# Optimization experiments

Measured on AMD Instinct MI355X. Metric: run time of the kernel, lower is better.

## Reference

```python
import jax, jax.numpy as jnp
import numpy as np

EPS = 1e-6

def rms_norm(x, w):
    # x: (..., hd), w: (hd,)
    norm = jax.lax.rsqrt(jnp.mean(x * x, axis=-1, keepdims=True) + EPS)
    return x * norm * w

def rotate_half(x):
    x1, x2 = jnp.split(x, 2, axis=-1)
    return jnp.concatenate((-x2, x1), axis=-1)

def setup_inputs() -> dict:
    key = jax.random.key(0)
    ks = jax.random.split(key, 5)
    B, L, C, H = 8, 1024, 1024, 16
    hd = C // H
    x = jax.random.normal(ks[0], (B, L, C), dtype=jnp.float32)
    # RoPE tables (realistic: derived from angles; any broadcastable table works)
    pos = jnp.arange(L, dtype=jnp.float32)[:, None]
    inv_freq = 1.0 / (10000.0 ** (jnp.arange(0, hd, 2, dtype=jnp.float32) / hd))
    ang = pos * inv_freq[None, :]              # (L, hd/2)
    ang = jnp.concatenate([ang, ang], axis=-1) # (L, hd)
    cos = jnp.cos(ang)
    sin = jnp.sin(ang)
    w_qkv = jax.random.normal(ks[1], (3 * C, C), dtype=jnp.float32) * (C ** -0.5)
    w_proj = jax.random.normal(ks[2], (C, C), dtype=jnp.float32) * (C ** -0.5)
    q_norm_w = jnp.ones((hd,), dtype=jnp.float32)
    k_norm_w = jnp.ones((hd,), dtype=jnp.float32)
    return {"x": x, "cos": cos, "sin": sin, "w_qkv": w_qkv, "w_proj": w_proj,
            "q_norm_w": q_norm_w, "k_norm_w": k_norm_w}

def reference(x, cos, sin, w_qkv, w_proj, q_norm_w, k_norm_w):
    B, L, C = x.shape
    H = 16
    hd = C // H
    # qkv: torch Linear(bias=False) -> x @ W^T, W: (3C, C)
    qkv = jnp.einsum('blc,dc->bld', x, w_qkv)             # (B, L, 3C)
    qkv = qkv.reshape(B, L, 3, H, hd).transpose(2, 0, 3, 1, 4)  # (3, B, H, L, hd)
    q, k, v = qkv[0], qkv[1], qkv[2]
    q = rms_norm(q, q_norm_w)
    k = rms_norm(k, k_norm_w)
    # RoPE: cos/sin (L, hd) broadcast over (B, H, L, hd)
    q = q * cos + rotate_half(q) * sin
    k = k * cos + rotate_half(k) * sin
    scale = 1.0 / np.sqrt(hd).astype(np.float32)
    attn = jnp.einsum('bhqd,bhkd->bhqk', q, k) * scale    # (B, H, L, L)
    attn = jax.nn.softmax(attn, axis=-1)
    out = jnp.einsum('bhqk,bhkd->bhqd', attn, v)          # (B, H, L, hd)
    out = out.transpose(0, 2, 1, 3).reshape(B, L, C)
    return jnp.einsum('blc,dc->bld', out, w_proj)
```

## Files before the change

kernel.cpp:

```cpp
#include <hip/hip_runtime.h>
#include <hip/hip_bf16.h>
#include <stdint.h>

typedef uint16_t u16;
typedef uint32_t u32;
typedef __attribute__((ext_vector_type(8))) short bv8;
typedef __attribute__((ext_vector_type(4))) float f32x4;
typedef __attribute__((ext_vector_type(16))) float f32x16;
typedef __attribute__((ext_vector_type(2))) u32 u32x2;

#define MFMA(a,b,c)   __builtin_amdgcn_mfma_f32_16x16x32_bf16((a),(b),(c),0,0,0)
#define MFMA32(a,b,c) __builtin_amdgcn_mfma_f32_32x32x16_bf16((a),(b),(c),0,0,0)

__device__ __forceinline__ float bf2f(u16 v){ u32 x=(u32)v<<16; float f; __builtin_memcpy(&f,&x,4); return f; }
__device__ __forceinline__ u16 f2bf(float f){ u32 x; __builtin_memcpy(&x,&f,4); x += 0x7fffu + ((x>>16)&1u); return (u16)(x>>16); }
__device__ __forceinline__ u32 cvtpk_bf16(float lo, float hi){
  u32 r; asm("v_cvt_pk_bf16_f32 %0, %1, %2" : "=v"(r) : "v"(lo), "v"(hi)); return r;
}
__device__ __forceinline__ float exp2_fast(float x){
  float r; asm("v_exp_f32 %0, %1" : "=v"(r) : "v"(x)); return r;
}
__device__ __forceinline__ float rcp_fast(float x){
  float r; asm("v_rcp_f32 %0, %1" : "=v"(r) : "v"(x)); return r;
}

__device__ __forceinline__ void gl_lds16(const u16* g, u16* l){
  __builtin_amdgcn_global_load_lds((const __attribute__((address_space(1))) u32*)g,
                                   (__attribute__((address_space(3))) u32*)l, 16, 0, 0);
}

__global__ __launch_bounds__(256) void cvt3(const float* __restrict__ x, const float* __restrict__ wq,
                                            const float* __restrict__ wp, u16* __restrict__ dst){
  const long NA = 1048576, NB = 393216, NC = 131072;
  long i = (long)blockIdx.x*256 + threadIdx.x;
  long stride = (long)gridDim.x*256;
  for(; i < NA+NB+NC; i += stride){
    const float* s;
    if(i < NA)            s = x  + i*8;
    else if(i < NA+NB)    s = wq + (i-NA)*8;
    else                  s = wp + (i-NA-NB)*8;
    f32x4 a = *(const f32x4*)(s);
    f32x4 b = *(const f32x4*)(s + 4);
    bv8 o;
    #pragma unroll
    for(int j=0;j<4;j++) o[j]   = (short)f2bf(a[j]);
    #pragma unroll
    for(int j=0;j<4;j++) o[4+j] = (short)f2bf(b[j]);
    *(bv8*)(dst + i*8) = o;
  }
}

template<int MODE>
__global__ __launch_bounds__(256,2) void gemm_bt(const u16* __restrict__ A, const u16* __restrict__ B,
                                                 void* __restrict__ Cv, int M, int N, int K,
                                                 const float* __restrict__ cosT,
                                                 const float* __restrict__ sinT,
                                                 const float* __restrict__ qw,
                                                 const float* __restrict__ kw){
  __shared__ __align__(16) u16 As[128*64];
  __shared__ __align__(16) u16 Bs[128*64];
  int nwg = gridDim.x;
  int wg  = (int)blockIdx.x;
  wg = (wg & 7)*(nwg>>3) + (wg>>3);
  int nn = N>>7;
  int tm = wg/nn, tn = wg - tm*nn;
  int rowbase = tm<<7, colbase = tn<<7;
  int t = threadIdx.x, lane = t&63, w = t>>6;
  int g = lane>>4, q16 = lane&15;
  int wr = w>>1, wc = w&1;

  f32x4 z = {0.f,0.f,0.f,0.f};
  f32x4 acc[4][4];
  #pragma unroll
  for(int i=0;i<4;i++)
    #pragma unroll
    for(int j=0;j<4;j++) acc[i][j]=z;

  for(int k0=0;k0<K;k0+=64){
    __syncthreads();
    #pragma unroll
    for(int i=0;i<4;i++){
      int s = ((w<<2)+i)*64 + lane;
      int row = s>>3;
      int ksl = (s&7) ^ (row&7);
      gl_lds16(A + (size_t)(rowbase+row)*K + k0 + ksl*8, (u16*)As + ((w<<2)+i)*512);
      gl_lds16(B + (size_t)(colbase+row)*K + k0 + ksl*8, (u16*)Bs + ((w<<2)+i)*512);
    }
    __syncthreads();
    #pragma unroll
    for(int eks=0;eks<2;eks++){
      bv8 af[4], bfr[4];
      #pragma unroll
      for(int mi=0;mi<4;mi++){
        int row = (wr<<6)+(mi<<4)+q16;
        af[mi] = *(const bv8*)(As + row*64 + ((((eks<<2)|g) ^ (row&7))<<3));
      }
      #pragma unroll
      for(int ni=0;ni<4;ni++){
        int row = (wc<<6)+(ni<<4)+q16;
        bfr[ni] = *(const bv8*)(Bs + row*64 + ((((eks<<2)|g) ^ (row&7))<<3));
      }
      #pragma unroll
      for(int mi=0;mi<4;mi++)
        #pragma unroll
        for(int ni=0;ni<4;ni++)
          acc[mi][ni] = MFMA(af[mi], bfr[ni], acc[mi][ni]);
    }
  }

  if(MODE==2 && colbase < 2048){
    int s = colbase>>10;
    const float* wsel = s ? kw : qw;
    int ch = colbase + (wc<<6);
    float qsc = s ? 1.0f : 0.1803368801111437f;
    float wv[4];
    #pragma unroll
    for(int ni=0;ni<4;ni++) wv[ni] = wsel[(ni<<4)|q16];
    #pragma unroll
    for(int mi=0;mi<4;mi++){
      #pragma unroll
      for(int r=0;r<4;r++){
        int row = rowbase + (wr<<6)+(mi<<4)+(g<<2)+r;
        int l = row & 1023;
        float y[4];
        float ss = 0.f;
        #pragma unroll
        for(int ni=0;ni<4;ni++){ y[ni]=acc[mi][ni][r]; ss += y[ni]*y[ni]; }
        ss += __shfl_xor(ss,1,64); ss += __shfl_xor(ss,2,64);
        ss += __shfl_xor(ss,4,64); ss += __shfl_xor(ss,8,64);
        float nrm = rsqrtf(ss*(1.f/64.f) + 1e-6f);
        #pragma unroll
        for(int ni=0;ni<4;ni++) y[ni] *= nrm * wv[ni];
        u16* cp = (u16*)Cv + (size_t)row*N + ch;
        #pragma unroll
        for(int ni=0;ni<4;ni++){
          int d = (ni<<4)|q16;
          float rot = (ni<2) ? -y[ni+2] : y[ni-2];
          float o = (y[ni]*cosT[l*64+d] + rot*sinT[l*64+d]) * qsc;
          cp[d] = f2bf(o);
        }
      }
    }
    return;
  }

  #pragma unroll
  for(int mi=0;mi<4;mi++){
    #pragma unroll
    for(int ni=0;ni<4;ni++){
      int row = rowbase + (wr<<6) + (mi<<4) + (g<<2);
      int col = colbase + (wc<<6) + (ni<<4) + q16;
      if(MODE==1){
        float* cp = (float*)Cv + (size_t)row*N + col;
        #pragma unroll
        for(int r=0;r<4;r++) cp[(size_t)r*N] = acc[mi][ni][r];
      } else {
        u16* cp = (u16*)Cv + (size_t)row*N + col;
        #pragma unroll
        for(int r=0;r<4;r++) cp[(size_t)r*N] = f2bf(acc[mi][ni][r]);
      }
    }
  }
}

__global__ __launch_bounds__(512,1) void fattn(const u16* __restrict__ qkv, u16* __restrict__ Out){
  __shared__ __align__(16) u16 Ks0[128*64];
  __shared__ __align__(16) u16 Ks1[128*64];
  __shared__ __align__(16) u16 Vt[2][64*128];

  int t = threadIdx.x, lane = t&63, w = t>>6;
  int ql = lane&31, h = lane>>5;
  int nwg = gridDim.x;
  int bid = (int)blockIdx.x;
  bid = (bid & 7)*(nwg>>3) + (bid>>3);
  int bh = bid >> 2, qt = bid & 3;
  int b = bh >> 4, hd = bh & 15;
  const u16* base = qkv + (size_t)b*1024*3072;
  int Qb = (qt<<8) + (w<<5);

  bv8 qf[4];
  {
    const u16* qp = base + (size_t)(Qb+ql)*3072 + hd*64 + (h<<3);
    qf[0] = *(const bv8*)(qp);
    qf[1] = *(const bv8*)(qp+16);
    qf[2] = *(const bv8*)(qp+32);
    qf[3] = *(const bv8*)(qp+48);
  }
  bv8 onesb;
  #pragma unroll
  for(int j=0;j<8;j++) onesb[j] = (short)0x3F80;

  f32x16 accO0, accO1, accL;
  #pragma unroll
  for(int r=0;r<16;r++){ accO0[r]=0.f; accO1[r]=0.f; accL[r]=0.f; }
  float m_run = -1e30f;

  bool vstage = (t < 256);
  int d0v = (t&7)<<3;
  int c4  = (t>>3)&31;
  int sV = c4>>1, halfV = c4&1, kvr = c4<<2;
  int d15b = (t&1)<<3;
  int vxt  = ((t>>1)&3)<<1;

  bv8 v0,v1,v2,v3;
  const u16* gV0 = base + (size_t)kvr*3072 + 2048 + hd*64 + d0v;

#define LDV(tl) if(vstage){ const u16* gV = gV0 + (size_t)(tl)*393216; \
    v0 = *(const bv8*)(gV);       v1 = *(const bv8*)(gV+3072); \
    v2 = *(const bv8*)(gV+6144);  v3 = *(const bv8*)(gV+9216); }

#define STV(buf) if(vstage){ \
    _Pragma("unroll") \
    for(int i=0;i<8;i++){ \
      int d = d0v + i; \
      u32x2 val; \
      val.x = (u32)(u16)v0[i] | ((u32)(u16)v1[i]<<16); \
      val.y = (u32)(u16)v2[i] | ((u32)(u16)v3[i]<<16); \
      *(u32x2*)((buf) + d*128 + ((((sV ^ (d15b+i) ^ vxt))<<3) + (halfV<<2))) = val; \
    } }

#define KDMA(tl, buf) { \
    _Pragma("unroll") \
    for(int i=0;i<2;i++){ \
      int si = ((w<<1)+i)*64 + lane; \
      int row = si>>3; \
      int esl = (si&7) ^ (row&7); \
      gl_lds16(base + (size_t)(((tl)<<7)+row)*3072 + 1024 + hd*64 + esl*8, (buf) + ((w<<1)+i)*512); \
    } }

  KDMA(0, (u16*)Ks0);
  LDV(0);
  STV(Vt[0]);
  LDV(1);

  int rx0 = (ql>>4)<<1;
  int dsw = ql & 15;

  for(int tile=0; tile<8; ++tile){
    u16* kcur = (tile&1) ? (u16*)Ks1 : (u16*)Ks0;
    u16* knxt = (tile&1) ? (u16*)Ks0 : (u16*)Ks1;
    u16* vcur = Vt[tile&1];
    u16* vnxt = Vt[(tile&1)^1];
    __syncthreads();
    if(tile<7) KDMA(tile+1, knxt);

    #pragma unroll
    for(int sub=0; sub<2; ++sub){
      f32x16 s0, s1;
      #pragma unroll
      for(int r=0;r<16;r++){ s0[r]=0.f; s1[r]=0.f; }
      int rowA = (sub<<6) + ql;
      int rowB = rowA + 32;
      __builtin_amdgcn_s_setprio(1);
      #pragma unroll
      for(int s=0;s<4;s++){
        bv8 ka = *(const bv8*)(kcur + rowA*64 + ((((s<<1)|h) ^ (rowA&7))<<3));
        bv8 kb = *(const bv8*)(kcur + rowB*64 + ((((s<<1)|h) ^ (rowB&7))<<3));
        s0 = MFMA32(ka, qf[s], s0);
        s1 = MFMA32(kb, qf[s], s1);
      }
      __builtin_amdgcn_s_setprio(0);

      if(sub==0){
        if(tile<7) STV(vnxt);
        if(tile<6) LDV(tile+2);
      }

      float rm = -1e30f;
      #pragma unroll
      for(int r=0;r<16;r++){ rm = fmaxf(rm, fmaxf(s0[r], s1[r])); }
      rm = fmaxf(rm, __shfl_xor(rm, 32, 64));
      if(__any(rm > m_run + 8.0f)){
        float mnew = fmaxf(m_run, rm);
        float fac = exp2_fast(m_run - mnew);
        m_run = mnew;
        #pragma unroll
        for(int r=0;r<16;r++){
          int qs = (r&3) + ((r>>2)<<3) + (h<<2);
          float fr = __shfl(fac, qs, 64);
          accO0[r] *= fr; accO1[r] *= fr; accL[r] *= fr;
        }
      }
      #pragma unroll
      for(int r=0;r<16;r++){
        s0[r] = exp2_fast(s0[r]-m_run);
        s1[r] = exp2_fast(s1[r]-m_run);
      }

      #pragma unroll
      for(int tt=0; tt<4; ++tt){
        int b0 = (tt&1)<<1;
        float a0,a1,a2,a3,b4,b5,b6,b7;
        if(tt<2){ a0=s0[4*b0+0]; a1=s0[4*b0+1]; a2=s0[4*b0+2]; a3=s0[4*b0+3];
                  b4=s0[4*b0+4]; b5=s0[4*b0+5]; b6=s0[4*b0+6]; b7=s0[4*b0+7]; }
        else    { a0=s1[4*b0+0]; a1=s1[4*b0+1]; a2=s1[4*b0+2]; a3=s1[4*b0+3];
                  b4=s1[4*b0+4]; b5=s1[4*b0+5]; b6=s1[4*b0+6]; b7=s1[4*b0+7]; }
        u32 Wlo0 = cvtpk_bf16(a0,a1), Wlo1 = cvtpk_bf16(a2,a3);
        u32 Whi0 = cvtpk_bf16(b4,b5), Whi1 = cvtpk_bf16(b6,b7);
        u32 X0 = h ? Wlo0 : Whi0;
        u32 X1 = h ? Wlo1 : Whi1;
        u32 x0 = (u32)__shfl_xor((int)X0, 32, 64);
        u32 x1 = (u32)__shfl_xor((int)X1, 32, 64);
        union { u32 u[4]; bv8 v; } pf;
        pf.u[0] = h ? x0 : Wlo0;
        pf.u[1] = h ? x1 : Wlo1;
        pf.u[2] = h ? Whi0 : x0;
        pf.u[3] = h ? Whi1 : x1;
        int vslot0 = (((sub<<3)+(tt<<1)+h) ^ dsw ^ rx0);
        bv8 vf0 = *(const bv8*)(vcur + ql*128 + (vslot0<<3));
        bv8 vf1 = *(const bv8*)(vcur + (32+ql)*128 + ((vslot0^4)<<3));
        __builtin_amdgcn_s_setprio(1);
        accO0 = MFMA32(pf.v, vf0, accO0);
        accO1 = MFMA32(pf.v, vf1, accO1);
        accL  = MFMA32(pf.v, onesb, accL);
        __builtin_amdgcn_s_setprio(0);
      }
    }
  }
  #pragma unroll
  for(int r=0;r<16;r++){
    int qs = (r&3) + ((r>>2)<<3) + (h<<2);
    float li = rcp_fast(accL[r]);
    size_t o = (size_t)(b*1024 + Qb + qs)*1024 + hd*64 + ql;
    Out[o]      = f2bf(accO0[r]*li);
    Out[o + 32] = f2bf(accO1[r]*li);
  }
#undef LDV
#undef STV
#undef KDMA
}

extern "C" void kernel_launch(void* const* d_in, const int* in_sizes, int n_in,
                              void* d_out, int out_size, void* d_ws, size_t ws_size,
                              hipStream_t stream) {
  const float* x      = (const float*)d_in[0];
  const float* cosT   = (const float*)d_in[1];
  const float* sinT   = (const float*)d_in[2];
  const float* w_qkv  = (const float*)d_in[3];
  const float* w_proj = (const float*)d_in[4];
  const float* qw     = (const float*)d_in[5];
  const float* kw     = (const float*)d_in[6];
  float* out = (float*)d_out;

  u16* xb     = (u16*)d_ws;
  u16* wqkvb  = xb     + (size_t) 8388608;
  u16* wprojb = wqkvb  + (size_t) 3145728;
  u16* qkv    = wprojb + (size_t) 1048576;
  u16* attn   = xb;

  cvt3<<<3072, 256, 0, stream>>>(x, w_qkv, w_proj, xb);

  gemm_bt<2><<<1536, 256, 0, stream>>>(xb, wqkvb, qkv, 8192, 3072, 1024,
                                       cosT, sinT, qw, kw);
  fattn   <<<512, 512, 0, stream>>>(qkv, attn);
  gemm_bt<1><<<512, 256, 0, stream>>>(attn, wprojb, out, 8192, 1024, 1024,
                                      nullptr, nullptr, nullptr, nullptr);
}
```

Before: 170.7 us.

## Process two 32-row query blocks per wave in flash attention, halving block size

The attention kernel now runs 256 threads per block instead of 512. Each wave handles 64 query rows as two independent 32-row groups (A and B), and both groups share every K and V fragment read from LDS. This cuts LDS read traffic per MFMA and lets all threads share the K DMA and V staging, with launch bounds allowing two blocks per CU. In exchange, register pressure roughly doubles for the accumulators and scores, which could cause spills or lower occupancy.

```diff
diff --git a/kernel.cpp b/kernel.cpp
--- a/kernel.cpp
+++ b/kernel.cpp
@@ -163,7 +163,7 @@
   }
 }
 
-__global__ __launch_bounds__(512,1) void fattn(const u16* __restrict__ qkv, u16* __restrict__ Out){
+__global__ __launch_bounds__(256,2) void fattn(const u16* __restrict__ qkv, u16* __restrict__ Out){
   __shared__ __align__(16) u16 Ks0[128*64];
   __shared__ __align__(16) u16 Ks1[128*64];
   __shared__ __align__(16) u16 Vt[2][64*128];
@@ -176,28 +176,32 @@
   int bh = bid >> 2, qt = bid & 3;
   int b = bh >> 4, hd = bh & 15;
   const u16* base = qkv + (size_t)b*1024*3072;
-  int Qb = (qt<<8) + (w<<5);
-
-  bv8 qf[4];
+  int Qb = (qt<<8) + (w<<6);
+
+  bv8 qfA[4], qfB[4];
   {
     const u16* qp = base + (size_t)(Qb+ql)*3072 + hd*64 + (h<<3);
-    qf[0] = *(const bv8*)(qp);
-    qf[1] = *(const bv8*)(qp+16);
-    qf[2] = *(const bv8*)(qp+32);
-    qf[3] = *(const bv8*)(qp+48);
+    qfA[0] = *(const bv8*)(qp);
+    qfA[1] = *(const bv8*)(qp+16);
+    qfA[2] = *(const bv8*)(qp+32);
+    qfA[3] = *(const bv8*)(qp+48);
+    const u16* qp2 = qp + (size_t)32*3072;
+    qfB[0] = *(const bv8*)(qp2);
+    qfB[1] = *(const bv8*)(qp2+16);
+    qfB[2] = *(const bv8*)(qp2+32);
+    qfB[3] = *(const bv8*)(qp2+48);
   }
   bv8 onesb;
   #pragma unroll
   for(int j=0;j<8;j++) onesb[j] = (short)0x3F80;
 
-  f32x16 accO0, accO1, accL;
-  #pragma unroll
-  for(int r=0;r<16;r++){ accO0[r]=0.f; accO1[r]=0.f; accL[r]=0.f; }
-  float m_run = -1e30f;
-
-  bool vstage = (t < 256);
+  f32x16 accO0A, accO1A, accO0B, accO1B, accLA, accLB;
+  #pragma unroll
+  for(int r=0;r<16;r++){ accO0A[r]=0.f; accO1A[r]=0.f; accO0B[r]=0.f; accO1B[r]=0.f; accLA[r]=0.f; accLB[r]=0.f; }
+  float mA = -1e30f, mB = -1e30f;
+
   int d0v = (t&7)<<3;
-  int c4  = (t>>3)&31;
+  int c4  = t>>3;
   int sV = c4>>1, halfV = c4&1, kvr = c4<<2;
   int d15b = (t&1)<<3;
   int vxt  = ((t>>1)&3)<<1;
@@ -205,11 +209,11 @@
   bv8 v0,v1,v2,v3;
   const u16* gV0 = base + (size_t)kvr*3072 + 2048 + hd*64 + d0v;
 
-#define LDV(tl) if(vstage){ const u16* gV = gV0 + (size_t)(tl)*393216; \
+#define LDV(tl) { const u16* gV = gV0 + (size_t)(tl)*393216; \
     v0 = *(const bv8*)(gV);       v1 = *(const bv8*)(gV+3072); \
     v2 = *(const bv8*)(gV+6144);  v3 = *(const bv8*)(gV+9216); }
 
-#define STV(buf) if(vstage){ \
+#define STV(buf) { \
     _Pragma("unroll") \
     for(int i=0;i<8;i++){ \
       int d = d0v + i; \
@@ -221,12 +225,48 @@
 
 #define KDMA(tl, buf) { \
     _Pragma("unroll") \
-    for(int i=0;i<2;i++){ \
-      int si = ((w<<1)+i)*64 + lane; \
+    for(int i=0;i<4;i++){ \
+      int si = ((w<<2)+i)*64 + lane; \
       int row = si>>3; \
       int esl = (si&7) ^ (row&7); \
-      gl_lds16(base + (size_t)(((tl)<<7)+row)*3072 + 1024 + hd*64 + esl*8, (buf) + ((w<<1)+i)*512); \
+      gl_lds16(base + (size_t)(((tl)<<7)+row)*3072 + 1024 + hd*64 + esl*8, (buf) + ((w<<2)+i)*512); \
     } }
+
+#define MKPF(SRC, pfv) { \
+      u32 Wlo0 = cvtpk_bf16(SRC[4*b0+0], SRC[4*b0+1]); \
+      u32 Wlo1 = cvtpk_bf16(SRC[4*b0+2], SRC[4*b0+3]); \
+      u32 Whi0 = cvtpk_bf16(SRC[4*b0+4], SRC[4*b0+5]); \
+      u32 Whi1 = cvtpk_bf16(SRC[4*b0+6], SRC[4*b0+7]); \
+      u32 X0 = h ? Wlo0 : Whi0; \
+      u32 X1 = h ? Wlo1 : Whi1; \
+      u32 x0 = (u32)__shfl_xor((int)X0, 32, 64); \
+      u32 x1 = (u32)__shfl_xor((int)X1, 32, 64); \
+      pfv.u[0] = h ? x0 : Wlo0; \
+      pfv.u[1] = h ? x1 : Wlo1; \
+      pfv.u[2] = h ? Whi0 : x0; \
+      pfv.u[3] = h ? Whi1 : x1; }
+
+#define SOFTMAX(S0_, S1_, M_, AO0_, AO1_, AL_) { \
+      float rm = -1e30f; \
+      _Pragma("unroll") \
+      for(int r=0;r<16;r++){ rm = fmaxf(rm, fmaxf(S0_[r], S1_[r])); } \
+      rm = fmaxf(rm, __shfl_xor(rm, 32, 64)); \
+      if(__any(rm > M_ + 8.0f)){ \
+        float mnew = fmaxf(M_, rm); \
+        float fac = exp2_fast(M_ - mnew); \
+        M_ = mnew; \
+        _Pragma("unroll") \
+        for(int r=0;r<16;r++){ \
+          int qs = (r&3) + ((r>>2)<<3) + (h<<2); \
+          float fr = __shfl(fac, qs, 64); \
+          AO0_[r] *= fr; AO1_[r] *= fr; AL_[r] *= fr; \
+        } \
+      } \
+      _Pragma("unroll") \
+      for(int r=0;r<16;r++){ \
+        S0_[r] = exp2_fast(S0_[r]-M_); \
+        S1_[r] = exp2_fast(S1_[r]-M_); \
+      } }
 
   KDMA(0, (u16*)Ks0);
   LDV(0);
@@ -246,9 +286,9 @@
 
     #pragma unroll
     for(int sub=0; sub<2; ++sub){
-      f32x16 s0, s1;
-      #pragma unroll
-      for(int r=0;r<16;r++){ s0[r]=0.f; s1[r]=0.f; }
+      f32x16 s0A, s1A, s0B, s1B;
+      #pragma unroll
+      for(int r=0;r<16;r++){ s0A[r]=0.f; s1A[r]=0.f; s0B[r]=0.f; s1B[r]=0.f; }
       int rowA = (sub<<6) + ql;
       int rowB = rowA + 32;
       __builtin_amdgcn_s_setprio(1);
@@ -256,8 +296,10 @@
       for(int s=0;s<4;s++){
         bv8 ka = *(const bv8*)(kcur + rowA*64 + ((((s<<1)|h) ^ (rowA&7))<<3));
         bv8 kb = *(const bv8*)(kcur + rowB*64 + ((((s<<1)|h) ^ (rowB&7))<<3));
-        s0 = MFMA32(ka, qf[s], s0);
-        s1 = MFMA32(kb, qf[s], s1);
+        s0A = MFMA32(ka, qfA[s], s0A);
+        s1A = MFMA32(kb, qfA[s], s1A);
+        s0B = MFMA32(ka, qfB[s], s0B);
+        s1B = MFMA32(kb, qfB[s], s1B);
       }
       __builtin_amdgcn_s_setprio(0);
 
@@ -266,53 +308,25 @@
         if(tile<6) LDV(tile+2);
       }
 
-      float rm = -1e30f;
-      #pragma unroll
-      for(int r=0;r<16;r++){ rm = fmaxf(rm, fmaxf(s0[r], s1[r])); }
-      rm = fmaxf(rm, __shfl_xor(rm, 32, 64));
-      if(__any(rm > m_run + 8.0f)){
-        float mnew = fmaxf(m_run, rm);
-        float fac = exp2_fast(m_run - mnew);
-        m_run = mnew;
-        #pragma unroll
-        for(int r=0;r<16;r++){
-          int qs = (r&3) + ((r>>2)<<3) + (h<<2);
-          float fr = __shfl(fac, qs, 64);
-          accO0[r] *= fr; accO1[r] *= fr; accL[r] *= fr;
-        }
-      }
-      #pragma unroll
-      for(int r=0;r<16;r++){
-        s0[r] = exp2_fast(s0[r]-m_run);
-        s1[r] = exp2_fast(s1[r]-m_run);
-      }
+      SOFTMAX(s0A, s1A, mA, accO0A, accO1A, accLA);
+      SOFTMAX(s0B, s1B, mB, accO0B, accO1B, accLB);
 
       #pragma unroll
       for(int tt=0; tt<4; ++tt){
         int b0 = (tt&1)<<1;
-        float a0,a1,a2,a3,b4,b5,b6,b7;
-        if(tt<2){ a0=s0[4*b0+0]; a1=s0[4*b0+1]; a2=s0[4*b0+2]; a3=s0[4*b0+3];
-                  b4=s0[4*b0+4]; b5=s0[4*b0+5]; b6=s0[4*b0+6]; b7=s0[4*b0+7]; }
-        else    { a0=s1[4*b0+0]; a1=s1[4*b0+1]; a2=s1[4*b0+2]; a3=s1[4*b0+3];
-                  b4=s1[4*b0+4]; b5=s1[4*b0+5]; b6=s1[4*b0+6]; b7=s1[4*b0+7]; }
-        u32 Wlo0 = cvtpk_bf16(a0,a1), Wlo1 = cvtpk_bf16(a2,a3);
-        u32 Whi0 = cvtpk_bf16(b4,b5), Whi1 = cvtpk_bf16(b6,b7);
-        u32 X0 = h ? Wlo0 : Whi0;
-        u32 X1 = h ? Wlo1 : Whi1;
-        u32 x0 = (u32)__shfl_xor((int)X0, 32, 64);
-        u32 x1 = (u32)__shfl_xor((int)X1, 32, 64);
-        union { u32 u[4]; bv8 v; } pf;
-        pf.u[0] = h ? x0 : Wlo0;
-        pf.u[1] = h ? x1 : Wlo1;
-        pf.u[2] = h ? Whi0 : x0;
-        pf.u[3] = h ? Whi1 : x1;
+        union { u32 u[4]; bv8 v; } pfA, pfB;
+        if(tt<2){ MKPF(s0A, pfA); MKPF(s0B, pfB); }
+        else    { MKPF(s1A, pfA); MKPF(s1B, pfB); }
         int vslot0 = (((sub<<3)+(tt<<1)+h) ^ dsw ^ rx0);
         bv8 vf0 = *(const bv8*)(vcur + ql*128 + (vslot0<<3));
         bv8 vf1 = *(const bv8*)(vcur + (32+ql)*128 + ((vslot0^4)<<3));
         __builtin_amdgcn_s_setprio(1);
-        accO0 = MFMA32(pf.v, vf0, accO0);
-        accO1 = MFMA32(pf.v, vf1, accO1);
-        accL  = MFMA32(pf.v, onesb, accL);
+        accO0A = MFMA32(pfA.v, vf0, accO0A);
+        accO1A = MFMA32(pfA.v, vf1, accO1A);
+        accO0B = MFMA32(pfB.v, vf0, accO0B);
+        accO1B = MFMA32(pfB.v, vf1, accO1B);
+        accLA  = MFMA32(pfA.v, onesb, accLA);
+        accLB  = MFMA32(pfB.v, onesb, accLB);
         __builtin_amdgcn_s_setprio(0);
       }
     }
@@ -320,14 +334,20 @@
   #pragma unroll
   for(int r=0;r<16;r++){
     int qs = (r&3) + ((r>>2)<<3) + (h<<2);
-    float li = rcp_fast(accL[r]);
-    size_t o = (size_t)(b*1024 + Qb + qs)*1024 + hd*64 + ql;
-    Out[o]      = f2bf(accO0[r]*li);
-    Out[o + 32] = f2bf(accO1[r]*li);
+    float liA = rcp_fast(accLA[r]);
+    float liB = rcp_fast(accLB[r]);
+    size_t oA = (size_t)(b*1024 + Qb + qs)*1024 + hd*64 + ql;
+    size_t oB = oA + (size_t)32*1024;
+    Out[oA]      = f2bf(accO0A[r]*liA);
+    Out[oA + 32] = f2bf(accO1A[r]*liA);
+    Out[oB]      = f2bf(accO0B[r]*liB);
+    Out[oB + 32] = f2bf(accO1B[r]*liB);
   }
 #undef LDV
 #undef STV
 #undef KDMA
+#undef MKPF
+#undef SOFTMAX
 }
 
 extern "C" void kernel_launch(void* const* d_in, const int* in_sizes, int n_in,
@@ -352,7 +372,7 @@
 
   gemm_bt<2><<<1536, 256, 0, stream>>>(xb, wqkvb, qkv, 8192, 3072, 1024,
                                        cosT, sinT, qw, kw);
-  fattn   <<<512, 512, 0, stream>>>(qkv, attn);
+  fattn   <<<512, 256, 0, stream>>>(qkv, attn);
   gemm_bt<1><<<512, 256, 0, stream>>>(attn, wprojb, out, 8192, 1024, 1024,
                                       nullptr, nullptr, nullptr, nullptr);
 }
```

New measurement: 183.7 us. +7.6%, slower.

## Replace QKV GEMM with 256x256-tile, 8-wave, double-buffered pipelined kernel

Applied to the files above, without the earlier changes.

Adds a dedicated QKV projection kernel using 256x256 output tiles, 512 threads, and double-buffered LDS fed by direct global-to-LDS loads, with explicit waitcnt/barrier scheduling and MFMA priority hints. The RMSNorm+RoPE epilogue is carried over. This aims to raise data reuse per tile and overlap global loads with MFMA work compared to the prior 128x128 single-buffer GEMM. It uses much more LDS and registers per block, and with only 384 blocks the occupancy and tail-wave balance may suffer. The old templated GEMM is simplified to only the fp32 output projection.

```diff
diff --git a/kernel.cpp b/kernel.cpp
--- a/kernel.cpp
+++ b/kernel.cpp
@@ -50,13 +50,152 @@
   }
 }
 
-template<int MODE>
+__global__ __launch_bounds__(512,1) void gemm8p(const u16* __restrict__ A, const u16* __restrict__ B,
+                                                u16* __restrict__ C,
+                                                const float* __restrict__ cosT,
+                                                const float* __restrict__ sinT,
+                                                const float* __restrict__ qw,
+                                                const float* __restrict__ kw){
+  const int K = 1024, N = 3072;
+  __shared__ __align__(16) u16 Ab[2][16384];
+  __shared__ __align__(16) u16 Bb[2][16384];
+  int nwg = gridDim.x;
+  int wg  = (int)blockIdx.x;
+  wg = (wg & 7)*(nwg>>3) + (wg>>3);
+  int tm = wg/12, tn = wg - tm*12;
+  int rowbase = tm<<8, colbase = tn<<8;
+  int t = threadIdx.x, lane = t&63, w = t>>6;
+  int g = lane>>4, q16 = lane&15;
+  int wm = w>>2, wn = w&3;
+
+  f32x4 z = {0.f,0.f,0.f,0.f};
+  f32x4 acc[8][4];
+  #pragma unroll
+  for(int i=0;i<8;i++)
+    #pragma unroll
+    for(int j=0;j<4;j++) acc[i][j]=z;
+
+  int srow = lane>>2;
+  int sslotL = lane&3;
+
+#define STGA(tile, kh) { \
+    _Pragma("unroll") \
+    for(int j=0;j<2;j++){ \
+      int row = (((w<<1)+j)<<4) + srow; \
+      int s = sslotL ^ ((row>>1)&3); \
+      gl_lds16(A + (size_t)(rowbase+row)*K + (tile)*64 + (kh)*32 + s*8, \
+               Ab[(tile)&1] + (kh)*8192 + (((w<<1)+j)<<9)); \
+    } }
+#define STGB(tile, kh) { \
+    _Pragma("unroll") \
+    for(int j=0;j<2;j++){ \
+      int row = (((w<<1)+j)<<4) + srow; \
+      int s = sslotL ^ ((row>>1)&3); \
+      gl_lds16(B + (size_t)(colbase+row)*K + (tile)*64 + (kh)*32 + s*8, \
+               Bb[(tile)&1] + (kh)*8192 + (((w<<1)+j)<<9)); \
+    } }
+
+  STGA(0,0); STGB(0,0); STGA(0,1); STGB(0,1); STGA(1,0); STGB(1,0);
+
+  bv8 af[8], bf[2];
+#define RD_A(p_, ks_) { \
+    _Pragma("unroll") \
+    for(int mi=0;mi<8;mi++){ \
+      int row = (wm<<7) + (mi<<4) + q16; \
+      af[mi] = *(const bv8*)(Ab[p_] + (ks_)*8192 + row*32 + ((g ^ ((row>>1)&3))<<3)); \
+    } }
+#define RD_B(p_, ks_, nh_) { \
+    _Pragma("unroll") \
+    for(int ni=0;ni<2;ni++){ \
+      int col = (wn<<6) + (nh_)*32 + (ni<<4) + q16; \
+      bf[ni] = *(const bv8*)(Bb[p_] + (ks_)*8192 + col*32 + ((g ^ ((col>>1)&3))<<3)); \
+    } }
+#define DO_MFMA(nh_) { \
+    __builtin_amdgcn_s_setprio(1); \
+    _Pragma("unroll") \
+    for(int mi=0;mi<8;mi++){ \
+      acc[mi][(nh_)*2+0] = MFMA(af[mi], bf[0], acc[mi][(nh_)*2+0]); \
+      acc[mi][(nh_)*2+1] = MFMA(af[mi], bf[1], acc[mi][(nh_)*2+1]); \
+    } \
+    __builtin_amdgcn_s_setprio(0); }
+
+  for(int tl=0; tl<16; ++tl){
+    int p = tl&1;
+    asm volatile("s_waitcnt vmcnt(8)" ::: "memory");
+    asm volatile("s_barrier" ::: "memory");
+    RD_A(p, 0); RD_B(p, 0, 0);
+    if(tl<15) STGA(tl+1, 1);
+    DO_MFMA(0);
+    asm volatile("s_barrier" ::: "memory");
+    RD_B(p, 0, 1);
+    if(tl<15) STGB(tl+1, 1);
+    DO_MFMA(1);
+    asm volatile("s_waitcnt vmcnt(8)" ::: "memory");
+    asm volatile("s_barrier" ::: "memory");
+    RD_A(p, 1); RD_B(p, 1, 0);
+    if(tl<14) STGA(tl+2, 0);
+    DO_MFMA(0);
+    asm volatile("s_barrier" ::: "memory");
+    RD_B(p, 1, 1);
+    if(tl<14) STGB(tl+2, 0);
+    DO_MFMA(1);
+  }
+
+  if(colbase < 2048){
+    int s = colbase>>10;
+    const float* wsel = s ? kw : qw;
+    int ch = colbase + (wn<<6);
+    float qsc = s ? 1.0f : 0.1803368801111437f;
+    float wv[4];
+    #pragma unroll
+    for(int ni=0;ni<4;ni++) wv[ni] = wsel[(ni<<4)|q16];
+    #pragma unroll
+    for(int mi=0;mi<8;mi++){
+      #pragma unroll
+      for(int r=0;r<4;r++){
+        int row = rowbase + (wm<<7)+(mi<<4)+(g<<2)+r;
+        int l = row & 1023;
+        float y[4];
+        float ss = 0.f;
+        #pragma unroll
+        for(int ni=0;ni<4;ni++){ y[ni]=acc[mi][ni][r]; ss += y[ni]*y[ni]; }
+        ss += __shfl_xor(ss,1,64); ss += __shfl_xor(ss,2,64);
+        ss += __shfl_xor(ss,4,64); ss += __shfl_xor(ss,8,64);
+        float nrm = rsqrtf(ss*(1.f/64.f) + 1e-6f);
+        #pragma unroll
+        for(int ni=0;ni<4;ni++) y[ni] *= nrm * wv[ni];
+        u16* cp = C + (size_t)row*N + ch;
+        #pragma unroll
+        for(int ni=0;ni<4;ni++){
+          int d = (ni<<4)|q16;
+          float rot = (ni<2) ? -y[ni+2] : y[ni-2];
+          float o = (y[ni]*cosT[l*64+d] + rot*sinT[l*64+d]) * qsc;
+          cp[d] = f2bf(o);
+        }
+      }
+    }
+  } else {
+    #pragma unroll
+    for(int mi=0;mi<8;mi++){
+      #pragma unroll
+      for(int ni=0;ni<4;ni++){
+        int row = rowbase + (wm<<7) + (mi<<4) + (g<<2);
+        int col = colbase + (wn<<6) + (ni<<4) + q16;
+        u16* cp = C + (size_t)row*N + col;
+        #pragma unroll
+        for(int r=0;r<4;r++) cp[(size_t)r*N] = f2bf(acc[mi][ni][r]);
+      }
+    }
+  }
+#undef STGA
+#undef STGB
+#undef RD_A
+#undef RD_B
+#undef DO_MFMA
+}
+
 __global__ __launch_bounds__(256,2) void gemm_bt(const u16* __restrict__ A, const u16* __restrict__ B,
-                                                 void* __restrict__ Cv, int M, int N, int K,
-                                                 const float* __restrict__ cosT,
-                                                 const float* __restrict__ sinT,
-                                                 const float* __restrict__ qw,
-                                                 const float* __restrict__ kw){
+                                                 float* __restrict__ C, int M, int N, int K){
   __shared__ __align__(16) u16 As[128*64];
   __shared__ __align__(16) u16 Bs[128*64];
   int nwg = gridDim.x;
@@ -107,58 +246,15 @@
           acc[mi][ni] = MFMA(af[mi], bfr[ni], acc[mi][ni]);
     }
   }
-
-  if(MODE==2 && colbase < 2048){
-    int s = colbase>>10;
-    const float* wsel = s ? kw : qw;
-    int ch = colbase + (wc<<6);
-    float qsc = s ? 1.0f : 0.1803368801111437f;
-    float wv[4];
-    #pragma unroll
-    for(int ni=0;ni<4;ni++) wv[ni] = wsel[(ni<<4)|q16];
-    #pragma unroll
-    for(int mi=0;mi<4;mi++){
-      #pragma unroll
-      for(int r=0;r<4;r++){
-        int row = rowbase + (wr<<6)+(mi<<4)+(g<<2)+r;
-        int l = row & 1023;
-        float y[4];
-        float ss = 0.f;
-        #pragma unroll
-        for(int ni=0;ni<4;ni++){ y[ni]=acc[mi][ni][r]; ss += y[ni]*y[ni]; }
-        ss += __shfl_xor(ss,1,64); ss += __shfl_xor(ss,2,64);
-        ss += __shfl_xor(ss,4,64); ss += __shfl_xor(ss,8,64);
-        float nrm = rsqrtf(ss*(1.f/64.f) + 1e-6f);
-        #pragma unroll
-        for(int ni=0;ni<4;ni++) y[ni] *= nrm * wv[ni];
-        u16* cp = (u16*)Cv + (size_t)row*N + ch;
-        #pragma unroll
-        for(int ni=0;ni<4;ni++){
-          int d = (ni<<4)|q16;
-          float rot = (ni<2) ? -y[ni+2] : y[ni-2];
-          float o = (y[ni]*cosT[l*64+d] + rot*sinT[l*64+d]) * qsc;
-          cp[d] = f2bf(o);
-        }
-      }
-    }
-    return;
-  }
-
   #pragma unroll
   for(int mi=0;mi<4;mi++){
     #pragma unroll
     for(int ni=0;ni<4;ni++){
       int row = rowbase + (wr<<6) + (mi<<4) + (g<<2);
       int col = colbase + (wc<<6) + (ni<<4) + q16;
-      if(MODE==1){
-        float* cp = (float*)Cv + (size_t)row*N + col;
-        #pragma unroll
-        for(int r=0;r<4;r++) cp[(size_t)r*N] = acc[mi][ni][r];
-      } else {
-        u16* cp = (u16*)Cv + (size_t)row*N + col;
-        #pragma unroll
-        for(int r=0;r<4;r++) cp[(size_t)r*N] = f2bf(acc[mi][ni][r]);
-      }
+      float* cp = C + (size_t)row*N + col;
+      #pragma unroll
+      for(int r=0;r<4;r++) cp[(size_t)r*N] = acc[mi][ni][r];
     }
   }
 }
@@ -350,9 +446,7 @@
 
   cvt3<<<3072, 256, 0, stream>>>(x, w_qkv, w_proj, xb);
 
-  gemm_bt<2><<<1536, 256, 0, stream>>>(xb, wqkvb, qkv, 8192, 3072, 1024,
-                                       cosT, sinT, qw, kw);
-  fattn   <<<512, 512, 0, stream>>>(qkv, attn);
-  gemm_bt<1><<<512, 256, 0, stream>>>(attn, wprojb, out, 8192, 1024, 1024,
-                                      nullptr, nullptr, nullptr, nullptr);
-}
+  gemm8p<<<384, 512, 0, stream>>>(xb, wqkvb, qkv, cosT, sinT, qw, kw);
+  fattn <<<512, 512, 0, stream>>>(qkv, attn);
+  gemm_bt<<<512, 256, 0, stream>>>(attn, wprojb, out, 8192, 1024, 1024);
+}
```

Measured after the change: 168.1 us. Within noise of the previous version (-1.5%).

## Double-buffer GEMM LDS tiles to overlap global loads with MFMA

Applied to the files above, without the earlier changes.

Splits the GEMM shared-memory tiles into two buffers. The next K-slice is issued into the alternate buffer while MFMAs run on the current one, which also cuts the barriers per K-step from two to one. It raises wave priority around the MFMA block with s_setprio. LDS use per block doubles to 64KB, which may limit occupancy, and correctness depends on the barrier waiting for the async global-to-LDS loads.

```diff
diff --git a/kernel.cpp b/kernel.cpp
--- a/kernel.cpp
+++ b/kernel.cpp
@@ -57,8 +57,8 @@
                                                  const float* __restrict__ sinT,
                                                  const float* __restrict__ qw,
                                                  const float* __restrict__ kw){
-  __shared__ __align__(16) u16 As[128*64];
-  __shared__ __align__(16) u16 Bs[128*64];
+  __shared__ __align__(16) u16 As[2][128*64];
+  __shared__ __align__(16) u16 Bs[2][128*64];
   int nwg = gridDim.x;
   int wg  = (int)blockIdx.x;
   wg = (wg & 7)*(nwg>>3) + (wg>>3);
@@ -68,6 +68,7 @@
   int t = threadIdx.x, lane = t&63, w = t>>6;
   int g = lane>>4, q16 = lane&15;
   int wr = w>>1, wc = w&1;
+  int nsteps = K>>6;
 
   f32x4 z = {0.f,0.f,0.f,0.f};
   f32x4 acc[4][4];
@@ -76,37 +77,45 @@
     #pragma unroll
     for(int j=0;j<4;j++) acc[i][j]=z;
 
-  for(int k0=0;k0<K;k0+=64){
+#define GSTAGE(step, p) { \
+    _Pragma("unroll") \
+    for(int i=0;i<4;i++){ \
+      int s = ((w<<2)+i)*64 + lane; \
+      int row = s>>3; \
+      int ksl = (s&7) ^ (row&7); \
+      gl_lds16(A + (size_t)(rowbase+row)*K + (step)*64 + ksl*8, (u16*)As[p] + ((w<<2)+i)*512); \
+      gl_lds16(B + (size_t)(colbase+row)*K + (step)*64 + ksl*8, (u16*)Bs[p] + ((w<<2)+i)*512); \
+    } }
+
+  GSTAGE(0, 0);
+
+  for(int st=0; st<nsteps; ++st){
+    int p = st&1;
     __syncthreads();
-    #pragma unroll
-    for(int i=0;i<4;i++){
-      int s = ((w<<2)+i)*64 + lane;
-      int row = s>>3;
-      int ksl = (s&7) ^ (row&7);
-      gl_lds16(A + (size_t)(rowbase+row)*K + k0 + ksl*8, (u16*)As + ((w<<2)+i)*512);
-      gl_lds16(B + (size_t)(colbase+row)*K + k0 + ksl*8, (u16*)Bs + ((w<<2)+i)*512);
-    }
-    __syncthreads();
+    if(st+1 < nsteps) GSTAGE(st+1, p^1);
     #pragma unroll
     for(int eks=0;eks<2;eks++){
       bv8 af[4], bfr[4];
       #pragma unroll
       for(int mi=0;mi<4;mi++){
         int row = (wr<<6)+(mi<<4)+q16;
-        af[mi] = *(const bv8*)(As + row*64 + ((((eks<<2)|g) ^ (row&7))<<3));
+        af[mi] = *(const bv8*)(As[p] + row*64 + ((((eks<<2)|g) ^ (row&7))<<3));
       }
       #pragma unroll
       for(int ni=0;ni<4;ni++){
         int row = (wc<<6)+(ni<<4)+q16;
-        bfr[ni] = *(const bv8*)(Bs + row*64 + ((((eks<<2)|g) ^ (row&7))<<3));
-      }
+        bfr[ni] = *(const bv8*)(Bs[p] + row*64 + ((((eks<<2)|g) ^ (row&7))<<3));
+      }
+      __builtin_amdgcn_s_setprio(1);
       #pragma unroll
       for(int mi=0;mi<4;mi++)
         #pragma unroll
         for(int ni=0;ni<4;ni++)
           acc[mi][ni] = MFMA(af[mi], bfr[ni], acc[mi][ni]);
+      __builtin_amdgcn_s_setprio(0);
     }
   }
+#undef GSTAGE
 
   if(MODE==2 && colbase < 2048){
     int s = colbase>>10;
@@ -352,7 +361,7 @@
 
   gemm_bt<2><<<1536, 256, 0, stream>>>(xb, wqkvb, qkv, 8192, 3072, 1024,
                                        cosT, sinT, qw, kw);
-  fattn   <<<512, 512, 0, stream>>>(qkv, attn);
+  fattn  <<<512, 512, 0, stream>>>(qkv, attn);
   gemm_bt<1><<<512, 256, 0, stream>>>(attn, wprojb, out, 8192, 1024, 1024,
                                       nullptr, nullptr, nullptr, nullptr);
 }
```

After: 164.3 us, median of 3. 1.04x faster.
